# Kernel tuning notes

Measured on AMD Instinct MI355X. Metric: run time of the kernel, lower is better.

The kernel has to match this reference:

```python
import jax, jax.numpy as jnp
import numpy as np

B, Q, P, K, E, H = 2, 2500, 2500, 2500, 256, 8
D = E // H
FF = 2 * E
EPS = 1e-5


def layernorm(x, g, b):
    mu = jnp.mean(x, axis=-1, keepdims=True)
    var = jnp.var(x, axis=-1, keepdims=True)
    return (x - mu) * jax.lax.rsqrt(var + EPS) * g + b


def mha(q_in, k_in, v_in, wq, wk, wv, scale):
    n, ql = q_in.shape[0], q_in.shape[1]
    q = (q_in @ wq).reshape(n, ql, H, D)
    k = (k_in @ wk).reshape(n, k_in.shape[1], H, D)
    v = (v_in @ wv).reshape(n, v_in.shape[1], H, D)
    scores = jnp.einsum('nqhd,nkhd->nhqk', q, k) / scale
    attn = jax.nn.softmax(scores, axis=-1)
    return jnp.einsum('nhqk,nkhd->nqhd', attn, v).reshape(n, ql, E)


def setup_inputs() -> dict:
    key = jax.random.key(0)
    ks = jax.random.split(key, 24)
    s = lambda i, shape, sc=0.02: jax.random.normal(ks[i], shape, dtype=jnp.float32) * sc
    return {
        'prev_seq': jax.random.normal(ks[0], (B, P, E), dtype=jnp.float32),
        'query': jax.random.normal(ks[1], (B, Q, E), dtype=jnp.float32),
        'img_ft': jax.random.normal(ks[2], (B, K, E), dtype=jnp.float32),
        't_wq': s(3, (E, E)), 't_wk': s(4, (E, E)), 't_wv': s(5, (E, E)),
        's_wq': s(6, (E, E)), 's_wk': s(7, (E, E)), 's_wv': s(8, (E, E)),
        's_wo': s(9, (E, E)), 's_bo': jnp.zeros((E,), jnp.float32),
        'n1_g': jnp.ones((E,), jnp.float32), 'n1_b': jnp.zeros((E,), jnp.float32),
        'n2_g': jnp.ones((E,), jnp.float32), 'n2_b': jnp.zeros((E,), jnp.float32),
        'n3_g': jnp.ones((E,), jnp.float32), 'n3_b': jnp.zeros((E,), jnp.float32),
        'ff_w1': s(10, (E, FF)), 'ff_b1': jnp.zeros((FF,), jnp.float32),
        'ff_w2': s(11, (FF, E)), 'ff_b2': jnp.zeros((E,), jnp.float32),
    }


def reference(prev_seq, query, img_ft, t_wq, t_wk, t_wv, s_wq, s_wk, s_wv,
              s_wo, s_bo, n1_g, n1_b, n2_g, n2_b, n3_g, n3_b,
              ff_w1, ff_b1, ff_w2, ff_b2):
    # Temporal self-attention: K/V from prev_seq, scale = sqrt(embed_size)
    attn = mha(query, prev_seq, prev_seq, t_wq, t_wk, t_wv, float(E) ** 0.5)
    x = layernorm(attn + query, n1_g, n1_b)
    # Spatial cross-attention: K/V from img_ft, scale = sqrt(head_dim), with fc_out
    cross = mha(x, img_ft, img_ft, s_wq, s_wk, s_wv, float(D) ** 0.5)
    cross = cross @ s_wo + s_bo
    x = layernorm(cross + x, n2_g, n2_b)
    # FFN: E -> 2E -> ReLU -> E
    ff = jax.nn.relu(x @ ff_w1 + ff_b1) @ ff_w2 + ff_b2
    return layernorm(ff + x, n3_g, n3_b)
```

## Files before the change

### kernel.cpp

```cpp
#include <hip/hip_runtime.h>
#include <hip/hip_bf16.h>
#include <stdint.h>


typedef __bf16 bf16_t;
typedef __bf16 bf16x8 __attribute__((ext_vector_type(8)));
typedef __bf16 bf16x4 __attribute__((ext_vector_type(4)));
typedef float  f32x4  __attribute__((ext_vector_type(4)));
typedef float  f32x16 __attribute__((ext_vector_type(16)));
typedef uint32_t u32;
typedef uint32_t u32x4 __attribute__((ext_vector_type(4)));

#define NB   2
#define SEQ  2500
#define EMB  256
#define NH   8
#define HD   32
#define MTOT (NB*SEQ)
#define KVSPLIT 5
#define SPLITLEN 500
#define NTILE 16

static __device__ __forceinline__ f32x4 mfma16(bf16x8 a, bf16x8 b, f32x4 c) {
  return __builtin_amdgcn_mfma_f32_16x16x32_bf16(a, b, c, 0, 0, 0);
}
static __device__ __forceinline__ f32x16 mfma32(bf16x8 a, bf16x8 b, f32x16 c) {
  return __builtin_amdgcn_mfma_f32_32x32x16_bf16(a, b, c, 0, 0, 0);
}
static __device__ __forceinline__ u32 pack2(float a, float b) {
  union { __bf16 h; unsigned short s; } x, y;
  x.h = (__bf16)a; y.h = (__bf16)b;
  return (u32)x.s | ((u32)y.s << 16);
}

__global__ __launch_bounds__(256) void prep_kernel(
    const float* s0, const float* s1, const float* s2, const float* s3,
    const float* s4, const float* s5, const float* s6, const float* s7,
    const float* s8, bf16_t* wt,
    const float* aq, const float* ap, const float* ai,
    bf16_t* dq, bf16_t* dp, bf16_t* di)
{
  int b = blockIdx.x;
  if (b < 176) {
    const float* src; int R, C, tl; size_t doff;
    if (b < 112) {
      int mi = b >> 4; tl = b & 15; R = 256; C = 256; doff = (size_t)mi * 65536;
      switch (mi) {
        case 0: src = s0; break; case 1: src = s1; break; case 2: src = s2; break;
        case 3: src = s3; break; case 4: src = s4; break; case 5: src = s5; break;
        default: src = s6;
      }
    } else if (b < 144) { tl = b - 112; R = 256; C = 512; doff = 458752; src = s7; }
    else                { tl = b - 144; R = 512; C = 256; doff = 589824; src = s8; }
    const int tpr = C >> 6;
    const int tr = tl / tpr, tc = tl % tpr;
    bf16_t* dst = wt + doff;
    #pragma unroll
    for (int i = 0; i < 16; ++i) {
      int lin = i * 256 + threadIdx.x;
      int lr = lin >> 6, lc = lin & 63;
      int rr = tr * 64 + lr, cc = tc * 64 + lc;
      dst[(size_t)cc * R + rr] = (__bf16)src[(size_t)rr * C + cc];
    }
    return;
  }
  int idx = b - 176;
  int t = idx / 313, r = idx % 313;
  const float* src = (t == 0) ? aq : (t == 1) ? ap : ai;
  bf16_t* dst = (t == 0) ? dq : (t == 1) ? dp : di;
  #pragma unroll
  for (int k = 0; k < 4; ++k) {
    int i = r * 1024 + k * 256 + threadIdx.x;
    if (i < 320000) {
      float4 v = ((const float4*)src)[i];
      bf16x4 o;
      o[0] = (__bf16)v.x; o[1] = (__bf16)v.y; o[2] = (__bf16)v.z; o[3] = (__bf16)v.w;
      ((bf16x4*)dst)[i] = o;
    }
  }
}

template<int K>
static __device__ __forceinline__ void gemm_body(
    const bf16_t* __restrict__ A, const bf16_t* __restrict__ Wt,
    const float* __restrict__ bias, bf16_t* __restrict__ Cout,
    int M, int N, int relu, float cscale, int bx, int by)
{
  const int tid = threadIdx.x;
  const int lane = tid & 63, wid = tid >> 6;
  const int l15 = lane & 15, g = lane >> 4;
  const int mbase = bx * 64 + wid * 16;
  const int nbase = by * 64;

  int arow = mbase + l15; if (arow > M - 1) arow = M - 1;
  const bf16_t* ap = A + (size_t)arow * K + g * 8;
  const bf16_t* bp = Wt + (size_t)(nbase + l15) * K + g * 8;

  f32x4 acc[4];
  #pragma unroll
  for (int j = 0; j < 4; ++j) acc[j] = (f32x4){0.f,0.f,0.f,0.f};

  #pragma unroll
  for (int kk = 0; kk < K; kk += 32) {
    bf16x8 a = *(const bf16x8*)(ap + kk);
    #pragma unroll
    for (int ct = 0; ct < 4; ++ct) {
      bf16x8 bfr = *(const bf16x8*)(bp + (size_t)ct * 16 * K + kk);
      acc[ct] = mfma16(a, bfr, acc[ct]);
    }
  }
  #pragma unroll
  for (int ct = 0; ct < 4; ++ct) {
    const int col = nbase + ct * 16 + l15;
    const float bv = bias ? bias[col] : 0.f;
    #pragma unroll
    for (int r = 0; r < 4; ++r) {
      const int row = mbase + g * 4 + r;
      if (row < M) {
        float v = acc[ct][r] * cscale + bv;
        if (relu) v = fmaxf(v, 0.f);
        Cout[(size_t)row * N + col] = (bf16_t)v;
      }
    }
  }
}

__global__ __launch_bounds__(256) void gemm_relu_kernel(
    const bf16_t* __restrict__ A, const bf16_t* __restrict__ Wt,
    const float* __restrict__ bias, bf16_t* __restrict__ Cout,
    int M, int N)
{
  gemm_body<256>(A, Wt, bias, Cout, M, N, 1, 1.f, blockIdx.x, blockIdx.y);
}

__global__ __launch_bounds__(256) void proj3_kernel(
    const bf16_t* A0, const bf16_t* W0, bf16_t* C0,
    const bf16_t* A1, const bf16_t* W1, bf16_t* C1,
    const bf16_t* A2, const bf16_t* W2, bf16_t* C2, float qsc)
{
  const bf16_t* A = (blockIdx.z == 0) ? A0 : (blockIdx.z == 1) ? A1 : A2;
  const bf16_t* W = (blockIdx.z == 0) ? W0 : (blockIdx.z == 1) ? W1 : W2;
  bf16_t* C = (blockIdx.z == 0) ? C0 : (blockIdx.z == 1) ? C1 : C2;
  const float cs = (blockIdx.z == 0) ? qsc : 1.f;
  gemm_body<256>(A, W, nullptr, C, MTOT, 256, 0, cs, blockIdx.x, blockIdx.y);
}

template<int K>
__global__ __launch_bounds__(256) void gemm_ln_kernel(
    const bf16_t* __restrict__ A, const bf16_t* __restrict__ Wt,
    const float* __restrict__ bias, const bf16_t* __restrict__ resid,
    const float* __restrict__ gw, const float* __restrict__ bw,
    bf16_t* __restrict__ OutB, float* __restrict__ OutF, int M)
{
  __shared__ float red[16][4][2];
  const int tid = threadIdx.x;
  const int lane = tid & 63, wid = tid >> 6;
  const int l15 = lane & 15, g = lane >> 4;
  const int mbase = blockIdx.x * 16;
  const int nbase = wid * 64;

  int arow = mbase + l15; if (arow > M - 1) arow = M - 1;
  const bf16_t* ap = A + (size_t)arow * K + g * 8;
  const bf16_t* bp = Wt + (size_t)(nbase + l15) * K + g * 8;

  f32x4 acc[4];
  #pragma unroll
  for (int j = 0; j < 4; ++j) acc[j] = (f32x4){0.f,0.f,0.f,0.f};

  #pragma unroll
  for (int kk = 0; kk < K; kk += 32) {
    bf16x8 a = *(const bf16x8*)(ap + kk);
    #pragma unroll
    for (int ct = 0; ct < 4; ++ct) {
      bf16x8 bfr = *(const bf16x8*)(bp + (size_t)ct * 16 * K + kk);
      acc[ct] = mfma16(a, bfr, acc[ct]);
    }
  }

  float x[4][4];
  float xs[4] = {0.f,0.f,0.f,0.f}, xq[4] = {0.f,0.f,0.f,0.f};
  #pragma unroll
  for (int ct = 0; ct < 4; ++ct) {
    const int col = nbase + ct * 16 + l15;
    const float bv = bias[col];
    #pragma unroll
    for (int r = 0; r < 4; ++r) {
      int row = mbase + g * 4 + r; if (row > M - 1) row = M - 1;
      float v = acc[ct][r] + bv + (float)resid[(size_t)row * EMB + col];
      x[ct][r] = v;
      xs[r] += v; xq[r] += v * v;
    }
  }
  #pragma unroll
  for (int r = 0; r < 4; ++r) {
    #pragma unroll
    for (int m = 1; m < 16; m <<= 1) {
      xs[r] += __shfl_xor(xs[r], m);
      xq[r] += __shfl_xor(xq[r], m);
    }
  }
  if (l15 == 0) {
    #pragma unroll
    for (int r = 0; r < 4; ++r) {
      red[g * 4 + r][wid][0] = xs[r];
      red[g * 4 + r][wid][1] = xq[r];
    }
  }
  __syncthreads();
  #pragma unroll
  for (int r = 0; r < 4; ++r) {
    const int rl = g * 4 + r;
    const float S = red[rl][0][0] + red[rl][1][0] + red[rl][2][0] + red[rl][3][0];
    const float Q = red[rl][0][1] + red[rl][1][1] + red[rl][2][1] + red[rl][3][1];
    const float mean = S * (1.f / EMB);
    const float var = Q * (1.f / EMB) - mean * mean;
    const float rstd = rsqrtf(var + 1e-5f);
    const int row = mbase + rl;
    if (row < M) {
      #pragma unroll
      for (int ct = 0; ct < 4; ++ct) {
        const int col = nbase + ct * 16 + l15;
        const float y = (x[ct][r] - mean) * rstd * gw[col] + bw[col];
        if (OutF) OutF[(size_t)row * EMB + col] = y;
        else      OutB[(size_t)row * EMB + col] = (bf16_t)y;
      }
    }
  }
}

__global__ __launch_bounds__(256, 4) void attn_part_kernel(
    const bf16_t* __restrict__ Qm, const bf16_t* __restrict__ Km,
    const bf16_t* __restrict__ Vm, bf16_t* __restrict__ Op,
    float* __restrict__ Lp)
{
  __shared__ bf16_t Vt[4][32][40];

  const int tid = threadIdx.x;
  const int lane = tid & 63, wid = tid >> 6;
  const int q32 = lane & 31, hi = lane >> 5;

  const int n = blockIdx.x;
  const int vid = (n & 7) * 200 + (n >> 3);
  const int grp = vid / 20;
  const int sub = vid - grp * 20;
  const int bh = grp / 5;
  const int split = grp - bh * 5;

  const size_t qoff = (size_t)(bh >> 3) * SEQ * EMB + (bh & 7) * HD;
  const int kv_begin = split * SPLITLEN;
  const int kv_end = kv_begin + SPLITLEN;

  const int qbase = sub * 128 + wid * 32;
  const int qr = min(qbase + q32, SEQ - 1);
  const bf16x8 qfa = *(const bf16x8*)(Qm + qoff + (size_t)qr * EMB + hi * 8);
  const bf16x8 qfb = *(const bf16x8*)(Qm + qoff + (size_t)qr * EMB + 16 + hi * 8);

  f32x16 accA = {}, accB = {};
  float lsum = 0.f;

  const int skv = tid >> 3;
  const int sd0 = (tid & 7) << 2;
  const int scc = (skv + ((sd0 >> 3) << 3)) & 31;

  const bf16_t* kp = Km + qoff + (size_t)(kv_begin + q32) * EMB + hi * 8;
  const bf16_t* vp = Vm + qoff + (size_t)(kv_begin + skv) * EMB + sd0;

  bf16x4 vA = *(const bf16x4*)vp;
  bf16x4 vB = *(const bf16x4*)(vp + 32 * EMB);
  bf16x8 kaA = *(const bf16x8*)kp;
  bf16x8 kbA = *(const bf16x8*)(kp + 16);
  bf16x8 kaB = *(const bf16x8*)(kp + 32 * EMB);
  bf16x8 kbB = *(const bf16x8*)(kp + 32 * EMB + 16);
  kp += 64 * EMB;
  vp += 64 * EMB;

#define TREE16(dst, p)                                                         \
    {                                                                          \
      float t0 = p[0] + p[1],  t1 = p[2] + p[3];                               \
      float t2 = p[4] + p[5],  t3 = p[6] + p[7];                               \
      float t4 = p[8] + p[9],  t5 = p[10] + p[11];                             \
      float t6 = p[12] + p[13], t7 = p[14] + p[15];                            \
      float u0 = t0 + t1, u1 = t2 + t3, u2 = t4 + t5, u3 = t6 + t7;            \
      dst = (u0 + u1) + (u2 + u3);                                             \
    }

#define SOFTPACK(p, f1, f2)                                                    \
    {                                                                          \
      u32 w0 = pack2(p[0], p[1]),   w1 = pack2(p[2], p[3]);                    \
      u32 w2 = pack2(p[4], p[5]),   w3 = pack2(p[6], p[7]);                    \
      u32 w4 = pack2(p[8], p[9]),   w5 = pack2(p[10], p[11]);                  \
      u32 w6 = pack2(p[12], p[13]), w7 = pack2(p[14], p[15]);                  \
      asm("v_permlane32_swap_b32 %0, %1" : "+v"(w0), "+v"(w2));                \
      asm("v_permlane32_swap_b32 %0, %1" : "+v"(w1), "+v"(w3));                \
      asm("v_permlane32_swap_b32 %0, %1" : "+v"(w4), "+v"(w6));                \
      asm("v_permlane32_swap_b32 %0, %1" : "+v"(w5), "+v"(w7));                \
      f1.x = w0; f1.y = w1; f1.z = w2; f1.w = w3;                              \
      f2.x = w4; f2.y = w5; f2.z = w6; f2.w = w7;                              \
    }

#define ATTN_PAIR(P, MASKED, PREFETCH)                                         \
  {                                                                            \
    const int bufA = ((P) & 1) << 1, bufB = bufA + 1;                          \
    _Pragma("unroll")                                                          \
    for (int j = 0; j < 4; ++j) {                                              \
      Vt[bufA][sd0 + j][scc] = vA[j];                                          \
      Vt[bufB][sd0 + j][scc] = vB[j];                                          \
    }                                                                          \
    bf16x4 vAn, vBn; bf16x8 kaAn, kbAn, kaBn, kbBn;                            \
    if (PREFETCH) {                                                            \
      vAn = *(const bf16x4*)vp;                                                \
      vBn = *(const bf16x4*)(vp + 32 * EMB);                                   \
      kaAn = *(const bf16x8*)kp;                                               \
      kbAn = *(const bf16x8*)(kp + 16);                                        \
      kaBn = *(const bf16x8*)(kp + 32 * EMB);                                  \
      kbBn = *(const bf16x8*)(kp + 32 * EMB + 16);                             \
      kp += 64 * EMB; vp += 64 * EMB;                                          \
    }                                                                          \
    f32x16 sA = {}, sB = {};                                                   \
    sA = mfma32(kaA, qfa, sA);                                                 \
    sB = mfma32(kaB, qfa, sB);                                                 \
    sA = mfma32(kbA, qfb, sA);                                                 \
    sB = mfma32(kbB, qfb, sB);                                                 \
    float pA[16], pB[16];                                                      \
    _Pragma("unroll")                                                          \
    for (int r = 0; r < 16; ++r) {                                             \
      pA[r] = __builtin_amdgcn_exp2f(sA[r]);                                   \
      pB[r] = __builtin_amdgcn_exp2f(sB[r]);                                   \
    }                                                                          \
    if (MASKED) {                                                              \
      const int kv0m = kv_begin + ((((P) << 1) + 1) << 5);                     \
      _Pragma("unroll")                                                        \
      for (int r = 0; r < 16; ++r) {                                           \
        const int kvg = kv0m + (r & 3) + ((r >> 2) << 3) + hi * 4;             \
        if (kvg >= kv_end) pB[r] = 0.f;                                        \
      }                                                                        \
    }                                                                          \
    float psA, psB;                                                            \
    TREE16(psA, pA)                                                            \
    TREE16(psB, pB)                                                            \
    lsum += psA + psB;                                                         \
    u32x4 f1A, f2A, f1B, f2B;                                                  \
    SOFTPACK(pA, f1A, f2A)                                                     \
    SOFTPACK(pB, f1B, f2B)                                                     \
    __syncthreads();                                                           \
    const int c1 = ((hi + (q32 >> 3)) & 3) << 3;                               \
    const int c2 = ((2 + hi + (q32 >> 3)) & 3) << 3;                           \
    bf16x8 vf1A = *(const bf16x8*)&Vt[bufA][q32][c1];                          \
    bf16x8 vf2A = *(const bf16x8*)&Vt[bufA][q32][c2];                          \
    bf16x8 vf1B = *(const bf16x8*)&Vt[bufB][q32][c1];                          \
    bf16x8 vf2B = *(const bf16x8*)&Vt[bufB][q32][c2];                          \
    accA = mfma32(*(bf16x8*)&f1A, vf1A, accA);                                 \
    accB = mfma32(*(bf16x8*)&f1B, vf1B, accB);                                 \
    accA = mfma32(*(bf16x8*)&f2A, vf2A, accA);                                 \
    accB = mfma32(*(bf16x8*)&f2B, vf2B, accB);                                 \
    if (PREFETCH) {                                                            \
      kaA = kaAn; kbA = kbAn; kaB = kaBn; kbB = kbBn;                          \
      vA = vAn; vB = vBn;                                                      \
    }                                                                          \
  }

  #pragma unroll
  for (int P = 0; P < 7; ++P) ATTN_PAIR(P, 0, 1)
  ATTN_PAIR(7, 1, 0)
#undef ATTN_PAIR
#undef SOFTPACK
#undef TREE16

  lsum += __shfl_xor(lsum, 32);
  const size_t pbase = ((size_t)split * 16 + bh) * SEQ;
  #pragma unroll
  for (int r = 0; r < 16; ++r) {
    const int q = qbase + (r & 3) + ((r >> 2) << 3) + hi * 4;
    if (q < SEQ) Op[(pbase + q) * 32 + q32] = (bf16_t)(accA[r] + accB[r]);
  }
  if (lane < 32) {
    const int q = qbase + lane;
    if (q < SEQ) Lp[pbase + q] = lsum;
  }
}

__global__ __launch_bounds__(256) void merge_kernel(
    const bf16_t* __restrict__ Op, const float* __restrict__ Lp,
    const bf16_t* __restrict__ resid, const float* __restrict__ gw,
    const float* __restrict__ bw, bf16_t* __restrict__ out, int doLN)
{
  const int lane = threadIdx.x & 63, wid = threadIdx.x >> 6;
  const int row = blockIdx.x * 4 + wid;
  const int b = row / SEQ, q = row - b * SEQ;
  const int h = lane >> 3, dl = (lane & 7) * 4;
  const int bh = b * 8 + h;

  float L = 0.f;
  float acc[4] = {0.f, 0.f, 0.f, 0.f};
  #pragma unroll
  for (int s = 0; s < KVSPLIT; ++s) {
    const size_t pb = ((size_t)s * 16 + bh) * SEQ + q;
    L += Lp[pb];
    bf16x4 ov = *(const bf16x4*)(Op + pb * 32 + dl);
    #pragma unroll
    for (int j = 0; j < 4; ++j) acc[j] += (float)ov[j];
  }
  const float invL = 1.f / L;
  const size_t base = (size_t)row * EMB + lane * 4;
  if (!doLN) {
    bf16x4 ov;
    #pragma unroll
    for (int j = 0; j < 4; ++j) ov[j] = (__bf16)(acc[j] * invL);
    *(bf16x4*)(out + base) = ov;
    return;
  }
  bf16x4 rv = *(const bf16x4*)(resid + base);
  float x[4], s = 0.f, sq = 0.f;
  #pragma unroll
  for (int j = 0; j < 4; ++j) {
    x[j] = acc[j] * invL + (float)rv[j];
    s += x[j]; sq += x[j] * x[j];
  }
  #pragma unroll
  for (int m = 1; m < 64; m <<= 1) { s += __shfl_xor(s, m); sq += __shfl_xor(sq, m); }
  const float mean = s * (1.f / EMB);
  const float var = sq * (1.f / EMB) - mean * mean;
  const float rstd = rsqrtf(var + 1e-5f);
  float4 gv = *(const float4*)(gw + lane * 4);
  float4 bv = *(const float4*)(bw + lane * 4);
  bf16x4 ov;
  ov[0] = (__bf16)((x[0] - mean) * rstd * gv.x + bv.x);
  ov[1] = (__bf16)((x[1] - mean) * rstd * gv.y + bv.y);
  ov[2] = (__bf16)((x[2] - mean) * rstd * gv.z + bv.z);
  ov[3] = (__bf16)((x[3] - mean) * rstd * gv.w + bv.w);
  *(bf16x4*)(out + base) = ov;
}

extern "C" void kernel_launch(void* const* d_in, const int* in_sizes, int n_in,
                              void* d_out, int out_size, void* d_ws, size_t ws_size,
                              hipStream_t stream)
{
  (void)in_sizes; (void)n_in; (void)out_size; (void)ws_size;
  const float* prev  = (const float*)d_in[0];
  const float* query = (const float*)d_in[1];
  const float* img   = (const float*)d_in[2];
  const float* t_wq  = (const float*)d_in[3];
  const float* t_wk  = (const float*)d_in[4];
  const float* t_wv  = (const float*)d_in[5];
  const float* s_wq  = (const float*)d_in[6];
  const float* s_wk  = (const float*)d_in[7];
  const float* s_wv  = (const float*)d_in[8];
  const float* s_wo  = (const float*)d_in[9];
  const float* s_bo  = (const float*)d_in[10];
  const float* n1g = (const float*)d_in[11];
  const float* n1b = (const float*)d_in[12];
  const float* n2g = (const float*)d_in[13];
  const float* n2b = (const float*)d_in[14];
  const float* n3g = (const float*)d_in[15];
  const float* n3b = (const float*)d_in[16];
  const float* ffw1 = (const float*)d_in[17];
  const float* ffb1 = (const float*)d_in[18];
  const float* ffw2 = (const float*)d_in[19];
  const float* ffb2 = (const float*)d_in[20];

  bf16_t* ws   = (bf16_t*)d_ws;
  bf16_t* WT   = ws;
  bf16_t* WTF1 = ws + 458752;
  bf16_t* WTF2 = ws + 589824;
  bf16_t* qbf = ws + 720896;
  bf16_t* pbf = qbf + 1280000;
  bf16_t* ibf = pbf + 1280000;
  bf16_t* qb = ibf + 1280000;
  bf16_t* kb = qb + 1280000;
  bf16_t* vb = kb + 1280000;
  bf16_t* ab = vb + 1280000;
  bf16_t* x1 = ab + 1280000;
  bf16_t* cb = x1 + 1280000;
  bf16_t* x2 = cb + 1280000;
  bf16_t* hb = x2 + 1280000;
  bf16_t* fb = hb + 2560000;
  float* outp = (float*)d_out;
  bf16_t* Op = cb;
  float*  Lp = (float*)pbf;

  const float log2e = 1.4426950408889634f;
  const float qscT = log2e * (1.f / 16.f);
  const float qscS = log2e * 0.17677669529663687f;

  dim3 blk(256);
  prep_kernel<<<1115, blk, 0, stream>>>(t_wq, t_wk, t_wv, s_wq, s_wk, s_wv,
                                        s_wo, ffw1, ffw2, ws,
                                        query, prev, img, qbf, pbf, ibf);

  dim3 gP(79, 4, 3), gG512(79, 8);
  proj3_kernel<<<gP, blk, 0, stream>>>(qbf, WT, qb,
                                       pbf, WT + 65536, kb,
                                       pbf, WT + 131072, vb, qscT);
  attn_part_kernel<<<1600, blk, 0, stream>>>(qb, kb, vb, Op, Lp);
  merge_kernel<<<1250, blk, 0, stream>>>(Op, Lp, qbf, n1g, n1b, x1, 1);
  proj3_kernel<<<gP, blk, 0, stream>>>(x1,  WT + 196608, qb,
                                       ibf, WT + 262144, kb,
                                       ibf, WT + 327680, vb, qscS);
  attn_part_kernel<<<1600, blk, 0, stream>>>(qb, kb, vb, Op, Lp);
  merge_kernel<<<1250, blk, 0, stream>>>(Op, Lp, nullptr, nullptr, nullptr, ab, 0);
  gemm_ln_kernel<256><<<313, blk, 0, stream>>>(ab, WT + 393216, s_bo, x1,
                                               n2g, n2b, x2, nullptr, MTOT);
  gemm_relu_kernel<<<gG512, blk, 0, stream>>>(x2, WTF1, ffb1, hb, MTOT, 512);
  gemm_ln_kernel<512><<<313, blk, 0, stream>>>(hb, WTF2, ffb2, x2,
                                               n3g, n3b, nullptr, outp, MTOT);
  (void)fb;
}
```

Baseline: 192.4 us.

## Process two 32-query tiles per wave in attention to reuse K/V fragments

Each wave in the split-KV attention kernel now handles 64 queries (two 32-row tiles) instead of 32. The K fragments loaded from global memory and the V tiles transposed through shared memory are reused for both tiles. This halves the grid to 800 blocks and halves K/V traffic and LDS staging per query. It doubles the accumulator and score registers, so launch bounds drop to 2 blocks per SM, which lowers occupancy and latency hiding.

```diff
diff --git a/kernel.cpp b/kernel.cpp
--- a/kernel.cpp
+++ b/kernel.cpp
@@ -228,7 +228,7 @@
   }
 }
 
-__global__ __launch_bounds__(256, 4) void attn_part_kernel(
+__global__ __launch_bounds__(256, 2) void attn_part_kernel(
     const bf16_t* __restrict__ Qm, const bf16_t* __restrict__ Km,
     const bf16_t* __restrict__ Vm, bf16_t* __restrict__ Op,
     float* __restrict__ Lp)
@@ -240,9 +240,9 @@
   const int q32 = lane & 31, hi = lane >> 5;
 
   const int n = blockIdx.x;
-  const int vid = (n & 7) * 200 + (n >> 3);
-  const int grp = vid / 20;
-  const int sub = vid - grp * 20;
+  const int vid = (n & 7) * 100 + (n >> 3);
+  const int grp = vid / 10;
+  const int sub = vid - grp * 10;
   const int bh = grp / 5;
   const int split = grp - bh * 5;
 
@@ -250,13 +250,16 @@
   const int kv_begin = split * SPLITLEN;
   const int kv_end = kv_begin + SPLITLEN;
 
-  const int qbase = sub * 128 + wid * 32;
-  const int qr = min(qbase + q32, SEQ - 1);
-  const bf16x8 qfa = *(const bf16x8*)(Qm + qoff + (size_t)qr * EMB + hi * 8);
-  const bf16x8 qfb = *(const bf16x8*)(Qm + qoff + (size_t)qr * EMB + 16 + hi * 8);
-
-  f32x16 accA = {}, accB = {};
-  float lsum = 0.f;
+  const int qbase = sub * 256 + wid * 64;
+  const int qrX = min(qbase + q32, SEQ - 1);
+  const int qrY = min(qbase + 32 + q32, SEQ - 1);
+  const bf16x8 qfaX = *(const bf16x8*)(Qm + qoff + (size_t)qrX * EMB + hi * 8);
+  const bf16x8 qfbX = *(const bf16x8*)(Qm + qoff + (size_t)qrX * EMB + 16 + hi * 8);
+  const bf16x8 qfaY = *(const bf16x8*)(Qm + qoff + (size_t)qrY * EMB + hi * 8);
+  const bf16x8 qfbY = *(const bf16x8*)(Qm + qoff + (size_t)qrY * EMB + 16 + hi * 8);
+
+  f32x16 accAX = {}, accBX = {}, accAY = {}, accBY = {};
+  float lsumX = 0.f, lsumY = 0.f;
 
   const int skv = tid >> 3;
   const int sd0 = (tid & 7) << 2;
@@ -296,6 +299,19 @@
       asm("v_permlane32_swap_b32 %0, %1" : "+v"(w5), "+v"(w7));                \
       f1.x = w0; f1.y = w1; f1.z = w2; f1.w = w3;                              \
       f2.x = w4; f2.y = w5; f2.z = w6; f2.w = w7;                              \
+    }
+
+#define EXPALL(p, s) _Pragma("unroll")                                         \
+    for (int r = 0; r < 16; ++r) p[r] = __builtin_amdgcn_exp2f(s[r]);
+
+#define MASKB(p, P)                                                            \
+    {                                                                          \
+      const int kv0m = kv_begin + ((((P) << 1) + 1) << 5);                     \
+      _Pragma("unroll")                                                        \
+      for (int r = 0; r < 16; ++r) {                                           \
+        const int kvg = kv0m + (r & 3) + ((r >> 2) << 3) + hi * 4;             \
+        if (kvg >= kv_end) p[r] = 0.f;                                         \
+      }                                                                        \
     }
 
 #define ATTN_PAIR(P, MASKED, PREFETCH)                                         \
@@ -316,32 +332,26 @@
       kbBn = *(const bf16x8*)(kp + 32 * EMB + 16);                             \
       kp += 64 * EMB; vp += 64 * EMB;                                          \
     }                                                                          \
-    f32x16 sA = {}, sB = {};                                                   \
-    sA = mfma32(kaA, qfa, sA);                                                 \
-    sB = mfma32(kaB, qfa, sB);                                                 \
-    sA = mfma32(kbA, qfb, sA);                                                 \
-    sB = mfma32(kbB, qfb, sB);                                                 \
-    float pA[16], pB[16];                                                      \
-    _Pragma("unroll")                                                          \
-    for (int r = 0; r < 16; ++r) {                                             \
-      pA[r] = __builtin_amdgcn_exp2f(sA[r]);                                   \
-      pB[r] = __builtin_amdgcn_exp2f(sB[r]);                                   \
-    }                                                                          \
-    if (MASKED) {                                                              \
-      const int kv0m = kv_begin + ((((P) << 1) + 1) << 5);                     \
-      _Pragma("unroll")                                                        \
-      for (int r = 0; r < 16; ++r) {                                           \
-        const int kvg = kv0m + (r & 3) + ((r >> 2) << 3) + hi * 4;             \
-        if (kvg >= kv_end) pB[r] = 0.f;                                        \
-      }                                                                        \
-    }                                                                          \
-    float psA, psB;                                                            \
-    TREE16(psA, pA)                                                            \
-    TREE16(psB, pB)                                                            \
-    lsum += psA + psB;                                                         \
-    u32x4 f1A, f2A, f1B, f2B;                                                  \
-    SOFTPACK(pA, f1A, f2A)                                                     \
-    SOFTPACK(pB, f1B, f2B)                                                     \
+    f32x16 sAX = {}, sBX = {}, sAY = {}, sBY = {};                             \
+    sAX = mfma32(kaA, qfaX, sAX);                                              \
+    sBX = mfma32(kaB, qfaX, sBX);                                              \
+    sAY = mfma32(kaA, qfaY, sAY);                                              \
+    sBY = mfma32(kaB, qfaY, sBY);                                              \
+    sAX = mfma32(kbA, qfbX, sAX);                                              \
+    sBX = mfma32(kbB, qfbX, sBX);                                              \
+    sAY = mfma32(kbA, qfbY, sAY);                                              \
+    sBY = mfma32(kbB, qfbY, sBY);                                              \
+    float pAX[16], pBX[16], pAY[16], pBY[16];                                  \
+    EXPALL(pAX, sAX) EXPALL(pBX, sBX) EXPALL(pAY, sAY) EXPALL(pBY, sBY)        \
+    if (MASKED) { MASKB(pBX, P) MASKB(pBY, P) }                                \
+    float ps0, ps1, ps2, ps3;                                                  \
+    TREE16(ps0, pAX) TREE16(ps1, pBX) TREE16(ps2, pAY) TREE16(ps3, pBY)        \
+    lsumX += ps0 + ps1; lsumY += ps2 + ps3;                                    \
+    u32x4 f1AX, f2AX, f1BX, f2BX, f1AY, f2AY, f1BY, f2BY;                      \
+    SOFTPACK(pAX, f1AX, f2AX)                                                  \
+    SOFTPACK(pBX, f1BX, f2BX)                                                  \
+    SOFTPACK(pAY, f1AY, f2AY)                                                  \
+    SOFTPACK(pBY, f1BY, f2BY)                                                  \
     __syncthreads();                                                           \
     const int c1 = ((hi + (q32 >> 3)) & 3) << 3;                               \
     const int c2 = ((2 + hi + (q32 >> 3)) & 3) << 3;                           \
@@ -349,10 +359,14 @@
     bf16x8 vf2A = *(const bf16x8*)&Vt[bufA][q32][c2];                          \
     bf16x8 vf1B = *(const bf16x8*)&Vt[bufB][q32][c1];                          \
     bf16x8 vf2B = *(const bf16x8*)&Vt[bufB][q32][c2];                          \
-    accA = mfma32(*(bf16x8*)&f1A, vf1A, accA);                                 \
-    accB = mfma32(*(bf16x8*)&f1B, vf1B, accB);                                 \
-    accA = mfma32(*(bf16x8*)&f2A, vf2A, accA);                                 \
-    accB = mfma32(*(bf16x8*)&f2B, vf2B, accB);                                 \
+    accAX = mfma32(*(bf16x8*)&f1AX, vf1A, accAX);                              \
+    accBX = mfma32(*(bf16x8*)&f1BX, vf1B, accBX);                              \
+    accAY = mfma32(*(bf16x8*)&f1AY, vf1A, accAY);                              \
+    accBY = mfma32(*(bf16x8*)&f1BY, vf1B, accBY);                              \
+    accAX = mfma32(*(bf16x8*)&f2AX, vf2A, accAX);                              \
+    accBX = mfma32(*(bf16x8*)&f2BX, vf2B, accBX);                              \
+    accAY = mfma32(*(bf16x8*)&f2AY, vf2A, accAY);                              \
+    accBY = mfma32(*(bf16x8*)&f2BY, vf2B, accBY);                              \
     if (PREFETCH) {                                                            \
       kaA = kaAn; kbA = kbAn; kaB = kaBn; kbB = kbBn;                          \
       vA = vAn; vB = vBn;                                                      \
@@ -365,17 +379,23 @@
 #undef ATTN_PAIR
 #undef SOFTPACK
 #undef TREE16
-
-  lsum += __shfl_xor(lsum, 32);
+#undef EXPALL
+#undef MASKB
+
+  lsumX += __shfl_xor(lsumX, 32);
+  lsumY += __shfl_xor(lsumY, 32);
   const size_t pbase = ((size_t)split * 16 + bh) * SEQ;
   #pragma unroll
   for (int r = 0; r < 16; ++r) {
-    const int q = qbase + (r & 3) + ((r >> 2) << 3) + hi * 4;
-    if (q < SEQ) Op[(pbase + q) * 32 + q32] = (bf16_t)(accA[r] + accB[r]);
+    const int qX = qbase + (r & 3) + ((r >> 2) << 3) + hi * 4;
+    const int qY = qX + 32;
+    if (qX < SEQ) Op[(pbase + qX) * 32 + q32] = (bf16_t)(accAX[r] + accBX[r]);
+    if (qY < SEQ) Op[(pbase + qY) * 32 + q32] = (bf16_t)(accAY[r] + accBY[r]);
   }
   if (lane < 32) {
-    const int q = qbase + lane;
-    if (q < SEQ) Lp[pbase + q] = lsum;
+    const int qX = qbase + lane, qY = qX + 32;
+    if (qX < SEQ) Lp[pbase + qX] = lsumX;
+    if (qY < SEQ) Lp[pbase + qY] = lsumY;
   }
 }
 
@@ -491,12 +511,12 @@
   proj3_kernel<<<gP, blk, 0, stream>>>(qbf, WT, qb,
                                        pbf, WT + 65536, kb,
                                        pbf, WT + 131072, vb, qscT);
-  attn_part_kernel<<<1600, blk, 0, stream>>>(qb, kb, vb, Op, Lp);
+  attn_part_kernel<<<800, blk, 0, stream>>>(qb, kb, vb, Op, Lp);
   merge_kernel<<<1250, blk, 0, stream>>>(Op, Lp, qbf, n1g, n1b, x1, 1);
   proj3_kernel<<<gP, blk, 0, stream>>>(x1,  WT + 196608, qb,
                                        ibf, WT + 262144, kb,
                                        ibf, WT + 327680, vb, qscS);
-  attn_part_kernel<<<1600, blk, 0, stream>>>(qb, kb, vb, Op, Lp);
+  attn_part_kernel<<<800, blk, 0, stream>>>(qb, kb, vb, Op, Lp);
   merge_kernel<<<1250, blk, 0, stream>>>(Op, Lp, nullptr, nullptr, nullptr, ab, 0);
   gemm_ln_kernel<256><<<313, blk, 0, stream>>>(ab, WT + 393216, s_bo, x1,
                                                n2g, n2b, x2, nullptr, MTOT);
```

Result: faster. 188.4 us (-2.1%).
